# Kernel optimization log

Hardware: AMD Instinct MI355X
Metric: run time of the kernel (lower is better)

The kernel has to match this reference:

```python
import jax, jax.numpy as jnp
import numpy as np

H, KV, HD = 16, 8, 128           # heads, kv heads, head_dim
THETA, EPS = 1.0e6, 1e-6         # rope theta, rmsnorm eps
QMAX = 127.0                     # symmetric int8


def qdq(x):
    """Symmetric int8 fake quant-dequant along last dim (per-token / per-out-channel)."""
    s = jnp.maximum(jnp.max(jnp.abs(x), axis=-1, keepdims=True) / QMAX, 1e-8)
    q = jnp.clip(jnp.round(x / s), -QMAX, QMAX) * s
    return x + jax.lax.stop_gradient(q - x)  # STE


def rms_norm(x, w):
    v = jnp.mean(jnp.square(x.astype(jnp.float32)), axis=-1, keepdims=True)
    return (x.astype(jnp.float32) * jax.lax.rsqrt(v + EPS)).astype(x.dtype) * w


def rotate_half(x):
    x1, x2 = jnp.split(x, 2, axis=-1)
    return jnp.concatenate([-x2, x1], axis=-1)


def setup_inputs() -> dict:
    key = jax.random.key(0)
    ks = jax.random.split(key, 6)
    B, S, D = 1, 2048, 2048
    return {
        "hidden_states": jax.random.normal(ks[0], (B, S, D), jnp.float32),
        "Wq": jax.random.normal(ks[1], (H * HD, D), jnp.float32) * 0.02,
        "Wk": jax.random.normal(ks[2], (KV * HD, D), jnp.float32) * 0.02,
        "Wv": jax.random.normal(ks[3], (KV * HD, D), jnp.float32) * 0.02,
        "Wo": jax.random.normal(ks[4], (D, H * HD), jnp.float32) * 0.02,
        "q_norm_w": jnp.ones((HD,), jnp.float32),
        "k_norm_w": jnp.ones((HD,), jnp.float32),
        "position_ids": jnp.arange(S, dtype=jnp.int32)[None, :],
    }


def reference(hidden_states, Wq, Wk, Wv, Wo, q_norm_w, k_norm_w, position_ids):
    B, S, D = hidden_states.shape
    xq = qdq(hidden_states)                                  # per-token act quant (shared input)
    q = (xq @ qdq(Wq).T).reshape(B, S, H, HD).transpose(0, 2, 1, 3)   # [B,H,S,hd]
    k = (xq @ qdq(Wk).T).reshape(B, S, KV, HD).transpose(0, 2, 1, 3)  # [B,KV,S,hd]
    v = (xq @ qdq(Wv).T).reshape(B, S, KV, HD).transpose(0, 2, 1, 3)

    q = rms_norm(q, q_norm_w)
    k = rms_norm(k, k_norm_w)

    # rotary embeddings
    inv = 1.0 / (THETA ** (jnp.arange(0, HD, 2, dtype=jnp.float32) / HD))
    freqs = position_ids.astype(jnp.float32)[..., None] * inv          # [B,S,hd/2]
    emb = jnp.concatenate([freqs, freqs], axis=-1)                     # [B,S,hd]
    cos = jnp.cos(emb)[:, None].astype(q.dtype)                        # [B,1,S,hd]
    sin = jnp.sin(emb)[:, None].astype(q.dtype)
    q = q * cos + rotate_half(q) * sin
    k = k * cos + rotate_half(k) * sin

    # qkt_matmul.quant_x1 / quant_x2
    q = qdq(q)
    k = qdq(k)

    # GQA repeat
    g = H // KV
    k = jnp.repeat(k, g, axis=1)
    v = jnp.repeat(v, g, axis=1)

    scores = jnp.einsum("bhqd,bhkd->bhqk", q, k) * (HD ** -0.5)       # [B,H,S,S]
    causal = jnp.tril(jnp.ones((S, S), bool))
    scores = jnp.where(causal[None, None], scores, jnp.float32(-1e9))
    p = jax.nn.softmax(scores.astype(jnp.float32), axis=-1).astype(q.dtype)

    # pv_matmul.quant_x1 / quant_x2
    p = qdq(p)
    v = qdq(v)
    attn = jnp.einsum("bhqk,bhkd->bhqd", p, v)                        # [B,H,S,hd]
    attn = attn.transpose(0, 2, 1, 3).reshape(B, S, H * HD)
    return qdq(attn) @ qdq(Wo).T
```

## Files before the change

kernel.cpp:

```cpp
#include <hip/hip_runtime.h>
#include <math.h>

#define NH 16
#define NKV 8
#define HDIM 128
#define SEQ 2048
#define DMODEL 2048

typedef int   v4i __attribute__((ext_vector_type(4)));
typedef float v4f __attribute__((ext_vector_type(4)));
typedef _Float16 v8h __attribute__((ext_vector_type(8)));

static constexpr float SM_SCALE = 0.08838834764831843f;

#define GLOBP(p) (__attribute__((address_space(1))) void*)(p)
#define LDSP(p)  (__attribute__((address_space(3))) void*)(p)
#define ASYNC16(g, l) __builtin_amdgcn_global_load_lds(GLOBP(g), LDSP(l), 16, 0, 0)


__device__ __forceinline__ unsigned short f2h_bits(float x) {
    _Float16 h = (_Float16)x;
    return __builtin_bit_cast(unsigned short, h);
}

__global__ __launch_bounds__(256) void quant_rope_k(const float* __restrict__ hidden,
        const float* __restrict__ Wq, const float* __restrict__ Wk,
        const float* __restrict__ Wv, const float* __restrict__ Wo,
        const int* __restrict__ pos_ids,
        signed char* __restrict__ out, float* __restrict__ scale,
        float* __restrict__ ct, float* __restrict__ st) {
    int p = blockIdx.x;
    if (p >= 512) {
        int t = (p - 512) * 4 + (threadIdx.x >> 6);
        int fi = threadIdx.x & 63;
        float inv = 1.0f / (float)pow(1.0e6, (double)fi / 64.0);
        float fr = (float)pos_ids[t] * inv;
        float sn, c;
        sincosf(fr, &sn, &c);
        ct[t * 64 + fi] = c;
        st[t * 64 + fi] = sn;
        return;
    }
    int row0g = p * 16;
    const float* in; int lr0;
    if (row0g < 2048)      { in = hidden; lr0 = row0g; }
    else if (row0g < 4096) { in = Wq; lr0 = row0g - 2048; }
    else if (row0g < 5120) { in = Wk; lr0 = row0g - 4096; }
    else if (row0g < 6144) { in = Wv; lr0 = row0g - 5120; }
    else                   { in = Wo; lr0 = row0g - 6144; }
    const int cols = 2048;
    int tid = threadIdx.x;
    __shared__ float srow[16];
    int r = tid >> 4, l16 = tid & 15;
    const float4* x4 = (const float4*)(in + (size_t)(lr0 + r) * cols);
    float amax = 0.f;
    for (int c4 = l16; c4 < (cols >> 2); c4 += 16) {
        float4 v = x4[c4];
        amax = fmaxf(amax, fmaxf(fmaxf(fabsf(v.x), fabsf(v.y)),
                                 fmaxf(fabsf(v.z), fabsf(v.w))));
    }
#pragma unroll
    for (int m = 1; m <= 8; m <<= 1) amax = fmaxf(amax, __shfl_xor(amax, m));
    if (l16 == 0) {
        float s = fmaxf(amax / 127.0f, 1e-8f);
        srow[r] = s;
        scale[row0g + r] = s;
    }
    __syncthreads();
    int total = (cols >> 4) * 16;
    size_t obase = (size_t)p * 32768;
    for (int idx = tid; idx < total; idx += 256) {
        int f = idx >> 6, q = (idx >> 4) & 3, rr = idx & 15;
        const float* src = in + (size_t)(lr0 + rr) * cols + f * 64 + q * 16;
        float s = srow[rr];
        unsigned int wds[4];
#pragma unroll
        for (int g = 0; g < 4; ++g) {
            float4 v = *(const float4*)(src + g * 4);
            int b0 = (int)fminf(fmaxf(rintf(v.x / s), -127.f), 127.f);
            int b1 = (int)fminf(fmaxf(rintf(v.y / s), -127.f), 127.f);
            int b2 = (int)fminf(fmaxf(rintf(v.z / s), -127.f), 127.f);
            int b3 = (int)fminf(fmaxf(rintf(v.w / s), -127.f), 127.f);
            wds[g] = (b0 & 255) | ((b1 & 255) << 8) | ((b2 & 255) << 16) | ((b3 & 255) << 24);
        }
        *(uint4*)(out + obase + (size_t)idx * 16) =
            make_uint4(wds[0], wds[1], wds[2], wds[3]);
    }
}

__global__ __launch_bounds__(256) void row_quant_red_k(const float* __restrict__ attn2,
        const float* __restrict__ pp, const float* __restrict__ zb,
        signed char* __restrict__ out, float* __restrict__ scale) {
    int row0 = blockIdx.x * 16;
    bool corr = (row0 >= 1024);
    int tid = threadIdx.x;
    __shared__ float srow[16];
    __shared__ float spvt[16][17];
    if (corr) {
        int r = tid >> 4, h = tid & 15;
        int row = row0 + r;
        int t16 = (row >> 6) - 16, rr = row & 63;
        float z0 = zb[(((size_t)h * 16 + t16) * 2 + 0) * 64 + rr];
        float z1 = zb[(((size_t)h * 16 + t16) * 2 + 1) * 64 + rr];
        spvt[r][h] = fmaxf((1.0f / (z0 + z1)) / 127.0f, 1e-8f);
    }
    __syncthreads();
    int r = tid >> 4, l16 = tid & 15;
    int row = row0 + r;
    const float4* x4 = (const float4*)(attn2 + (size_t)row * 2048);
    size_t ppr = corr ? ((((size_t)(row >> 6) - 16) * 64 + (row & 63)) * 128) : 0;
    float amax = 0.f;
    for (int c4 = l16; c4 < 512; c4 += 16) {
        float4 v = x4[c4];
        if (corr) {
            int h = c4 >> 5;
            int j = (c4 & 31) * 4;
            float4 pv = *(const float4*)&pp[(size_t)h * 16 * 64 * 128 + ppr + j];
            float s = spvt[r][h];
            v.x = (v.x + pv.x) * s; v.y = (v.y + pv.y) * s;
            v.z = (v.z + pv.z) * s; v.w = (v.w + pv.w) * s;
        }
        amax = fmaxf(amax, fmaxf(fmaxf(fabsf(v.x), fabsf(v.y)),
                                 fmaxf(fabsf(v.z), fabsf(v.w))));
    }
#pragma unroll
    for (int m = 1; m <= 8; m <<= 1) amax = fmaxf(amax, __shfl_xor(amax, m));
    if (l16 == 0) {
        float s = fmaxf(amax / 127.0f, 1e-8f);
        srow[r] = s;
        scale[row0 + r] = s;
    }
    __syncthreads();
    size_t obase = ((size_t)(row0 >> 4) * 32) << 10;
    for (int idx = tid; idx < 2048; idx += 256) {
        int f = idx >> 6, q = (idx >> 4) & 3, rr16 = idx & 15;
        int rowb = row0 + rr16;
        int colb = f * 64 + q * 16;
        const float* src = attn2 + (size_t)rowb * 2048 + colb;
        float s = srow[rr16];
        int h = f >> 1;
        float sp = corr ? spvt[rr16][h] : 0.f;
        size_t ppb = corr ? ((size_t)h * 16 * 64 * 128
                     + (((size_t)(rowb >> 6) - 16) * 64 + (rowb & 63)) * 128 + (colb & 127)) : 0;
        unsigned int wds[4];
#pragma unroll
        for (int g = 0; g < 4; ++g) {
            float4 v = *(const float4*)(src + g * 4);
            if (corr) {
                float4 pv = *(const float4*)&pp[ppb + g * 4];
                v.x = (v.x + pv.x) * sp; v.y = (v.y + pv.y) * sp;
                v.z = (v.z + pv.z) * sp; v.w = (v.w + pv.w) * sp;
            }
            int b0 = (int)fminf(fmaxf(rintf(v.x / s), -127.f), 127.f);
            int b1 = (int)fminf(fmaxf(rintf(v.y / s), -127.f), 127.f);
            int b2 = (int)fminf(fmaxf(rintf(v.z / s), -127.f), 127.f);
            int b3 = (int)fminf(fmaxf(rintf(v.w / s), -127.f), 127.f);
            wds[g] = (b0 & 255) | ((b1 & 255) << 8) | ((b2 & 255) << 16) | ((b3 & 255) << 24);
        }
        *(uint4*)(out + obase + (size_t)idx * 16) =
            make_uint4(wds[0], wds[1], wds[2], wds[3]);
    }
}

__global__ __launch_bounds__(256, 3) void gemm_o_k(const signed char* __restrict__ A,
        const float* __restrict__ sa, const signed char* __restrict__ B,
        const float* __restrict__ sb, float* __restrict__ C, int M, int N, int K) {
    __shared__ __align__(16) signed char lsA[3][8192];
    __shared__ __align__(16) signed char lsB[3][4096];
    int tid = threadIdx.x;
    int w = tid >> 6, l = tid & 63;
    int wr = w >> 1, wc = w & 1;
    int lrow = l & 15;
    int m0 = blockIdx.y * 128, n0 = blockIdx.x * 64;
    int kb6 = K >> 6;
    v4i acc[4][2];
#pragma unroll
    for (int i = 0; i < 4; ++i)
#pragma unroll
        for (int j = 0; j < 2; ++j) acc[i][j] = (v4i){0, 0, 0, 0};

    auto stage = [&](int buf, int k6) {
#pragma unroll
        for (int a = 0; a < 2; ++a) {
            int f = a * 4 + w;
            ASYNC16(A + (((size_t)(((m0 >> 4) + f) * kb6 + k6)) << 10) + l * 16,
                    lsA[buf] + f * 1024);
        }
        ASYNC16(B + (((size_t)(((n0 >> 4) + w) * kb6 + k6)) << 10) + l * 16,
                lsB[buf] + w * 1024);
    };

    stage(0, 0);
    if (kb6 > 1) {
        stage(1, 1);
        asm volatile("s_waitcnt vmcnt(3)" ::: "memory");
    } else {
        asm volatile("s_waitcnt vmcnt(0)" ::: "memory");
    }
    __builtin_amdgcn_s_barrier();
    for (int t = 0; t < kb6; ++t) {
        if (t + 2 < kb6) stage((t + 2) % 3, t + 2);
        int cur = t % 3;
        v4i af[4], bf[2];
#pragma unroll
        for (int i = 0; i < 4; ++i) af[i] = *(const v4i*)(lsA[cur] + (wr * 4 + i) * 1024 + l * 16);
#pragma unroll
        for (int j = 0; j < 2; ++j) bf[j] = *(const v4i*)(lsB[cur] + (wc * 2 + j) * 1024 + l * 16);
#pragma unroll
        for (int i = 0; i < 4; ++i)
#pragma unroll
            for (int j = 0; j < 2; ++j)
                acc[i][j] = __builtin_amdgcn_mfma_i32_16x16x64_i8(af[i], bf[j], acc[i][j], 0, 0, 0);
        if (t + 2 < kb6) asm volatile("s_waitcnt vmcnt(3)" ::: "memory");
        else             asm volatile("s_waitcnt vmcnt(0)" ::: "memory");
        __builtin_amdgcn_s_barrier();
    }
    int r0 = m0 + wr * 64, c0 = n0 + wc * 32;
    int lg = l >> 4;
    float sbv[2];
#pragma unroll
    for (int j = 0; j < 2; ++j) sbv[j] = sb[c0 + j * 16 + lrow];
#pragma unroll
    for (int i = 0; i < 4; ++i) {
        float4 s4 = *(const float4*)(sa + r0 + i * 16 + lg * 4);
        float sav[4] = {s4.x, s4.y, s4.z, s4.w};
#pragma unroll
        for (int j = 0; j < 2; ++j) {
#pragma unroll
            for (int reg = 0; reg < 4; ++reg) {
                int rr = r0 + i * 16 + lg * 4 + reg;
                C[(size_t)rr * N + c0 + j * 16 + lrow] = (float)acc[i][j][reg] * (sav[reg] * sbv[j]);
            }
        }
    }
}

__global__ __launch_bounds__(256, 2) void gemm_qkv_k(const signed char* __restrict__ A,
        const float* __restrict__ sa, const signed char* __restrict__ B,
        const float* __restrict__ sb,
        const float* __restrict__ qw, const float* __restrict__ kw,
        const float* __restrict__ ct, const float* __restrict__ st,
        signed char* __restrict__ q_i8, float* __restrict__ sq,
        signed char* __restrict__ k_i8, float* __restrict__ sk,
        unsigned short* __restrict__ vtT) {
    __shared__ __align__(16) char smem[68608];
    signed char (*lsA)[8192] = (signed char(*)[8192])smem;
    signed char (*lsB)[8192] = (signed char(*)[8192])(smem + 24576);
    float (*tile)[132] = (float(*)[132])smem;
    float* srow = (float*)(smem + 67584);
    int tid = threadIdx.x;
    int w = tid >> 6, l = tid & 63;
    int wr = w >> 1, wc = w & 1;
    int lrow = l & 15, lg = l >> 4;
    int m0 = blockIdx.y * 128, n0 = blockIdx.x * 128;
    const int kb6 = 32;
    v4i acc[4][4];
#pragma unroll
    for (int i = 0; i < 4; ++i)
#pragma unroll
        for (int j = 0; j < 4; ++j) acc[i][j] = (v4i){0, 0, 0, 0};

    auto stage = [&](int buf, int k6) {
#pragma unroll
        for (int a = 0; a < 2; ++a) {
            int f = a * 4 + w;
            ASYNC16(A + (((size_t)(((m0 >> 4) + f) * kb6 + k6)) << 10) + l * 16,
                    lsA[buf] + f * 1024);
            ASYNC16(B + (((size_t)(((n0 >> 4) + f) * kb6 + k6)) << 10) + l * 16,
                    lsB[buf] + f * 1024);
        }
    };

    stage(0, 0);
    stage(1, 1);
    asm volatile("s_waitcnt vmcnt(4)" ::: "memory");
    __builtin_amdgcn_s_barrier();
    for (int t = 0; t < kb6; ++t) {
        if (t + 2 < kb6) stage((t + 2) % 3, t + 2);
        int cur = t % 3;
        v4i af[4], bf[4];
#pragma unroll
        for (int i = 0; i < 4; ++i) af[i] = *(const v4i*)(lsA[cur] + (wr * 4 + i) * 1024 + l * 16);
#pragma unroll
        for (int j = 0; j < 4; ++j) bf[j] = *(const v4i*)(lsB[cur] + (wc * 4 + j) * 1024 + l * 16);
#pragma unroll
        for (int i = 0; i < 4; ++i)
#pragma unroll
            for (int j = 0; j < 4; ++j)
                acc[i][j] = __builtin_amdgcn_mfma_i32_16x16x64_i8(af[i], bf[j], acc[i][j], 0, 0, 0);
        if (t + 2 < kb6) asm volatile("s_waitcnt vmcnt(4)" ::: "memory");
        else             asm volatile("s_waitcnt vmcnt(0)" ::: "memory");
        __builtin_amdgcn_s_barrier();
    }
    {
        int c0 = n0 + wc * 64;
        float sbv[4];
#pragma unroll
        for (int j = 0; j < 4; ++j) sbv[j] = sb[c0 + j * 16 + lrow];
#pragma unroll
        for (int i = 0; i < 4; ++i) {
            float4 s4 = *(const float4*)(sa + m0 + wr * 64 + i * 16 + lg * 4);
            float sav[4] = {s4.x, s4.y, s4.z, s4.w};
#pragma unroll
            for (int j = 0; j < 4; ++j)
#pragma unroll
                for (int reg = 0; reg < 4; ++reg)
                    tile[wr * 64 + i * 16 + lg * 4 + reg][wc * 64 + j * 16 + lrow] =
                        (float)acc[i][j][reg] * (sav[reg] * sbv[j]);
        }
    }
    __syncthreads();
    int slot = n0 >> 7;
    if (slot < 24) {
        const float* wn = (slot < 16) ? qw : kw;
        signed char* dst8 = (slot < 16) ? q_i8 + (size_t)slot * (SEQ * 128)
                                        : k_i8 + (size_t)(slot - 16) * (SEQ * 128);
        float* sdst = (slot < 16) ? sq + (size_t)slot * SEQ : sk + (size_t)(slot - 16) * SEQ;
        float wn0 = wn[l], wn1 = wn[l + 64];
        for (int it = 0; it < 32; ++it) {
            int tl = it * 4 + w;
            int t = m0 + tl;
            float x0 = tile[tl][l];
            float x1 = tile[tl][l + 64];
            float ss = x0 * x0 + x1 * x1;
#pragma unroll
            for (int m = 1; m <= 32; m <<= 1) ss += __shfl_xor(ss, m);
            float rs = 1.0f / sqrtf(ss / 128.0f + 1e-6f);
            x0 = (x0 * rs) * wn0;
            x1 = (x1 * rs) * wn1;
            float cth = ct[t * 64 + l];
            float sth = st[t * 64 + l];
            float nx0 = x0 * cth - x1 * sth;
            float nx1 = x1 * cth + x0 * sth;
            float amax = fmaxf(fabsf(nx0), fabsf(nx1));
#pragma unroll
            for (int m = 1; m <= 32; m <<= 1) amax = fmaxf(amax, __shfl_xor(amax, m));
            float s = fmaxf(amax / 127.0f, 1e-8f);
            float q0 = fminf(fmaxf(rintf(nx0 / s), -127.f), 127.f);
            float q1 = fminf(fmaxf(rintf(nx1 / s), -127.f), 127.f);
            size_t ta0 = (size_t)(((t >> 4) * 2) << 10)
                       + (size_t)((((l >> 4) & 3) << 8) + ((t & 15) << 4) + (l & 15));
            dst8[ta0] = (signed char)(int)q0;
            dst8[ta0 + 1024] = (signed char)(int)q1;
            if (l == 0) sdst[t] = s;
        }
    } else {
        int kv = slot - 24;
        for (int it = 0; it < 32; ++it) {
            int tl = it * 4 + w;
            float x0 = tile[tl][l];
            float x1 = tile[tl][l + 64];
            float amax = fmaxf(fabsf(x0), fabsf(x1));
#pragma unroll
            for (int m = 1; m <= 32; m <<= 1) amax = fmaxf(amax, __shfl_xor(amax, m));
            if (l == 0) srow[tl] = fmaxf(amax / 127.0f, 1e-8f);
        }
        __syncthreads();
        int d = tid >> 1, th = (tid & 1) * 32;
        size_t base = (size_t)kv * (SEQ * 128);
#pragma unroll
        for (int kbl = 0; kbl < 2; ++kbl) {
            int kb = (m0 >> 6) + kbl;
#pragma unroll
            for (int j = 0; j < 32; j += 2) {
                int t64 = th + j;
                int tg = kbl * 64 + t64;
                float s0 = srow[tg], s1 = srow[tg + 1];
                float a = fminf(fmaxf(rintf(tile[tg][d] / s0), -127.f), 127.f) * s0;
                float b = fminf(fmaxf(rintf(tile[tg + 1][d] / s1), -127.f), 127.f) * s1;
                unsigned int ua = f2h_bits(a), ub = f2h_bits(b);
                int off = kb * 8192 + ((d >> 4) * 2 + ((t64 >> 5) & 1)) * 512
                        + (((d & 15) + (((t64 >> 3) & 3) << 4)) << 3) + (t64 & 7);
                *(unsigned int*)(vtT + base + off) = ua | (ub << 16);
            }
        }
    }
}

__global__ __launch_bounds__(256, 4) void attn_p1_k(const signed char* __restrict__ q_i8,
        const float* __restrict__ sq, const signed char* __restrict__ k_i8,
        const float* __restrict__ sk, float* __restrict__ mm) {
    int bx = blockIdx.x, hp = blockIdx.y;
    int qb = 31 - (bx >> 2), c = bx & 3;
    int nch = (qb + 8) >> 3;
    if (c >= nch) return;
    int q0 = qb * 64;
    int kb0 = c * 8, kb1 = min((c + 1) * 8, qb + 1);
    int tid = threadIdx.x, w = tid >> 6, l = tid & 63;
    int lrow = l & 15, lg = l >> 4;
    int h0 = hp * 2, h1 = h0 + 1;

    const signed char* qtA = q_i8 + (size_t)h0 * (SEQ * 128)
                           + ((size_t)((((q0 >> 4) + w) * 2)) << 10) + l * 16;
    const signed char* qtB = qtA + (size_t)(SEQ * 128);
    v4i qfA0 = *(const v4i*)(qtA), qfA1 = *(const v4i*)(qtA + 1024);
    v4i qfB0 = *(const v4i*)(qtB), qfB1 = *(const v4i*)(qtB + 1024);
    float4 sA = *(const float4*)(sq + (size_t)h0 * SEQ + q0 + w * 16 + lg * 4);
    float4 sB = *(const float4*)(sq + (size_t)h1 * SEQ + q0 + w * 16 + lg * 4);
    float sqrA[4] = {sA.x, sA.y, sA.z, sA.w};
    float sqrB[4] = {sB.x, sB.y, sB.z, sB.w};
    const signed char* kbase = k_i8 + (size_t)hp * (SEQ * 128);
    const float* skb = sk + (size_t)hp * SEQ;

    float mA[4], mB[4];
#pragma unroll
    for (int r = 0; r < 4; ++r) { mA[r] = -1e30f; mB[r] = -1e30f; }

    v4i ka[8], kn[8];
    float skc[4], skn[4];
    auto loadK = [&](v4i* dst, float* sdst, int k0) {
#pragma unroll
        for (int f = 0; f < 8; ++f)
            dst[f] = *(const v4i*)(kbase + ((size_t)((k0 >> 4) * 2 + f) << 10) + l * 16);
#pragma unroll
        for (int j = 0; j < 4; ++j) sdst[j] = skb[k0 + j * 16 + lrow];
    };

    loadK(ka, skc, kb0 * 64);
    for (int kb = kb0; kb < kb1; ++kb) {
        if (kb + 1 < kb1) loadK(kn, skn, (kb + 1) * 64);
        int k0 = kb * 64;
        v4i sciA[4], sciB[4];
#pragma unroll
        for (int j = 0; j < 4; ++j) {
            v4i z = {0, 0, 0, 0};
            v4i tA = __builtin_amdgcn_mfma_i32_16x16x64_i8(qfA0, ka[j * 2], z, 0, 0, 0);
            sciA[j] = __builtin_amdgcn_mfma_i32_16x16x64_i8(qfA1, ka[j * 2 + 1], tA, 0, 0, 0);
            v4i tB = __builtin_amdgcn_mfma_i32_16x16x64_i8(qfB0, ka[j * 2], z, 0, 0, 0);
            sciB[j] = __builtin_amdgcn_mfma_i32_16x16x64_i8(qfB1, ka[j * 2 + 1], tB, 0, 0, 0);
        }
#pragma unroll
        for (int reg = 0; reg < 4; ++reg) {
            int r = q0 + w * 16 + lg * 4 + reg;
#pragma unroll
            for (int j = 0; j < 4; ++j) {
                bool ok = (k0 + j * 16 + lrow <= r);
                float ss = skc[j] * SM_SCALE;
                float svA = ((float)sciA[j][reg] * sqrA[reg]) * ss;
                float svB = ((float)sciB[j][reg] * sqrB[reg]) * ss;
                mA[reg] = fmaxf(mA[reg], ok ? svA : -1e30f);
                mB[reg] = fmaxf(mB[reg], ok ? svB : -1e30f);
            }
        }
        if (kb + 1 < kb1) {
#pragma unroll
            for (int f = 0; f < 8; ++f) ka[f] = kn[f];
#pragma unroll
            for (int j = 0; j < 4; ++j) skc[j] = skn[j];
        }
    }
#pragma unroll
    for (int reg = 0; reg < 4; ++reg) {
#pragma unroll
        for (int mask = 1; mask <= 8; mask <<= 1) {
            mA[reg] = fmaxf(mA[reg], __shfl_xor(mA[reg], mask));
            mB[reg] = fmaxf(mB[reg], __shfl_xor(mB[reg], mask));
        }
    }
    if (lrow == 0) {
        size_t bA = ((size_t)(h0 * 32 + qb) * 4 + c) * 64;
        size_t bB = ((size_t)(h1 * 32 + qb) * 4 + c) * 64;
#pragma unroll
        for (int reg = 0; reg < 4; ++reg) {
            mm[bA + w * 16 + lg * 4 + reg] = mA[reg];
            mm[bB + w * 16 + lg * 4 + reg] = mB[reg];
        }
    }
}

__global__ __launch_bounds__(256, 2) void attn_p2_k(const signed char* __restrict__ q_i8,
        const float* __restrict__ sq, const signed char* __restrict__ k_i8,
        const float* __restrict__ sk, const unsigned short* __restrict__ vtT,
        const float* __restrict__ mm, float* __restrict__ attn2, float* __restrict__ pp,
        float* __restrict__ zb) {
    __shared__ __align__(16) unsigned short vlds[3][8192];
    __shared__ __align__(16) signed char klds[2][8192];
    __shared__ __align__(16) unsigned short plds[4096];
    __shared__ __align__(16) float slds[1024];
    int bx = blockIdx.x, hp = blockIdx.y;
    int qb = 31 - (bx >> 1), c = bx & 1;
    int nch2 = (qb >= 16) ? 2 : 1;
    if (c >= nch2) return;
    int q0 = qb * 64;
    int kb0 = c * 16, kb1 = min((c + 1) * 16, qb + 1);
    int tid = threadIdx.x, w = tid >> 6, l = tid & 63;
    int lrow = l & 15, lg = l >> 4;
    int h0 = hp * 2, h1 = h0 + 1;

    const signed char* qtA = q_i8 + (size_t)h0 * (SEQ * 128)
                           + ((size_t)((((q0 >> 4) + w) * 2)) << 10) + l * 16;
    const signed char* qtB = qtA + (size_t)(SEQ * 128);
    v4i qfA0 = *(const v4i*)(qtA), qfA1 = *(const v4i*)(qtA + 1024);
    v4i qfB0 = *(const v4i*)(qtB), qfB1 = *(const v4i*)(qtB + 1024);
    float4 sA = *(const float4*)(sq + (size_t)h0 * SEQ + q0 + w * 16 + lg * 4);
    float4 sB = *(const float4*)(sq + (size_t)h1 * SEQ + q0 + w * 16 + lg * 4);
    float sqrA[4] = {sA.x, sA.y, sA.z, sA.w};
    float sqrB[4] = {sB.x, sB.y, sB.z, sB.w};

    int nch1 = (qb + 8) >> 3;
    float mfA[4], mfB[4];
#pragma unroll
    for (int reg = 0; reg < 4; ++reg) {
        int r = w * 16 + lg * 4 + reg;
        float MA = -1e30f, MB = -1e30f;
        for (int c1 = 0; c1 < nch1; ++c1) {
            MA = fmaxf(MA, mm[((size_t)(h0 * 32 + qb) * 4 + c1) * 64 + r]);
            MB = fmaxf(MB, mm[((size_t)(h1 * 32 + qb) * 4 + c1) * 64 + r]);
        }
        mfA[reg] = MA; mfB[reg] = MB;
    }

    const signed char* kbase = k_i8 + (size_t)hp * (SEQ * 128);
    const float* skb = sk + (size_t)hp * SEQ;
    const unsigned short* vt = vtT + (size_t)hp * (SEQ * 128);

    auto issueV = [&](int kb) {
        unsigned short* vb = &vlds[kb % 3][0];
#pragma unroll
        for (int a = 0; a < 4; ++a) {
            int fv = a * 4 + w;
            ASYNC16(vt + (size_t)kb * 8192 + fv * 512 + l * 8, vb + fv * 512);
        }
    };
    auto issueK = [&](int kb) {
        signed char* kbuf = &klds[kb & 1][0];
#pragma unroll
        for (int a = 0; a < 2; ++a) {
            int f = a * 4 + w;
            ASYNC16(kbase + ((size_t)(kb * 8 + f) << 10) + l * 16, kbuf + f * 1024);
        }
    };

    v4f accA[8], accB[8];
#pragma unroll
    for (int jd = 0; jd < 8; ++jd) {
        accA[jd] = (v4f){0.f, 0.f, 0.f, 0.f};
        accB[jd] = (v4f){0.f, 0.f, 0.f, 0.f};
    }
    float ztA[4] = {0.f, 0.f, 0.f, 0.f};
    float ztB[4] = {0.f, 0.f, 0.f, 0.f};

    ASYNC16(skb + kb0 * 64 + w * 256 + l * 4, (char*)slds + w * 1024);
    issueK(kb0);
    issueV(kb0);
    if (kb0 + 1 < kb1) {
        issueV(kb0 + 1);
        asm volatile("s_waitcnt vmcnt(4)" ::: "memory");
    } else {
        asm volatile("s_waitcnt vmcnt(0)" ::: "memory");
    }
    __builtin_amdgcn_s_barrier();

    for (int kb = kb0; kb < kb1; ++kb) {
        int k0 = kb * 64;
        if (kb + 1 < kb1) issueK(kb + 1);
        if (kb + 2 < kb1) issueV(kb + 2);
        v4i ka[8];
#pragma unroll
        for (int f = 0; f < 8; ++f)
            ka[f] = *(const v4i*)(&klds[kb & 1][0] + f * 1024 + l * 16);
        float skc[4];
#pragma unroll
        for (int j = 0; j < 4; ++j) skc[j] = slds[(kb - kb0) * 64 + j * 16 + lrow];
        v4i sciA[4], sciB[4];
#pragma unroll
        for (int j = 0; j < 4; ++j) {
            v4i z = {0, 0, 0, 0};
            v4i tA = __builtin_amdgcn_mfma_i32_16x16x64_i8(qfA0, ka[j * 2], z, 0, 0, 0);
            sciA[j] = __builtin_amdgcn_mfma_i32_16x16x64_i8(qfA1, ka[j * 2 + 1], tA, 0, 0, 0);
            v4i tB = __builtin_amdgcn_mfma_i32_16x16x64_i8(qfB0, ka[j * 2], z, 0, 0, 0);
            sciB[j] = __builtin_amdgcn_mfma_i32_16x16x64_i8(qfB1, ka[j * 2 + 1], tB, 0, 0, 0);
        }
#pragma unroll
        for (int reg = 0; reg < 4; ++reg) {
            int rq = lg * 4 + reg;
            int r = q0 + w * 16 + rq;
#pragma unroll
            for (int j = 0; j < 4; ++j) {
                int cc = j * 16 + lrow;
                float pd = 0.f;
                if (k0 + cc <= r) {
                    float sv = ((float)sciA[j][reg] * (sqrA[reg] * skc[j])) * SM_SCALE;
                    float e = __expf(sv - mfA[reg]);
                    ztA[reg] += e;
                    pd = fminf(rintf(127.0f * e), 127.f);
                }
                plds[(w * 2 + (cc >> 5)) * 512 + (rq + 16 * ((cc >> 3) & 3)) * 8 + (cc & 7)] =
                    f2h_bits(pd);
            }
        }
        v8h pfA0 = *(const v8h*)(plds + (w * 2 + 0) * 512 + l * 8);
        v8h pfA1 = *(const v8h*)(plds + (w * 2 + 1) * 512 + l * 8);
#pragma unroll
        for (int reg = 0; reg < 4; ++reg) {
            int rq = lg * 4 + reg;
            int r = q0 + w * 16 + rq;
#pragma unroll
            for (int j = 0; j < 4; ++j) {
                int cc = j * 16 + lrow;
                float pd = 0.f;
                if (k0 + cc <= r) {
                    float sv = ((float)sciB[j][reg] * (sqrB[reg] * skc[j])) * SM_SCALE;
                    float e = __expf(sv - mfB[reg]);
                    ztB[reg] += e;
                    pd = fminf(rintf(127.0f * e), 127.f);
                }
                plds[(w * 2 + (cc >> 5)) * 512 + (rq + 16 * ((cc >> 3) & 3)) * 8 + (cc & 7)] =
                    f2h_bits(pd);
            }
        }
        v8h pfB0 = *(const v8h*)(plds + (w * 2 + 0) * 512 + l * 8);
        v8h pfB1 = *(const v8h*)(plds + (w * 2 + 1) * 512 + l * 8);
        const unsigned short* vb = &vlds[kb % 3][0];
#pragma unroll
        for (int jd = 0; jd < 8; ++jd) {
            v8h vh0 = *(const v8h*)(vb + (jd * 2 + 0) * 512 + l * 8);
            v8h vh1 = *(const v8h*)(vb + (jd * 2 + 1) * 512 + l * 8);
            v4f tA = accA[jd];
            tA = __builtin_amdgcn_mfma_f32_16x16x32_f16(pfA0, vh0, tA, 0, 0, 0);
            tA = __builtin_amdgcn_mfma_f32_16x16x32_f16(pfA1, vh1, tA, 0, 0, 0);
            accA[jd] = tA;
            v4f tB = accB[jd];
            tB = __builtin_amdgcn_mfma_f32_16x16x32_f16(pfB0, vh0, tB, 0, 0, 0);
            tB = __builtin_amdgcn_mfma_f32_16x16x32_f16(pfB1, vh1, tB, 0, 0, 0);
            accB[jd] = tB;
        }
        if (kb + 2 < kb1) asm volatile("s_waitcnt vmcnt(4)" ::: "memory");
        else              asm volatile("s_waitcnt vmcnt(0)" ::: "memory");
        __builtin_amdgcn_s_barrier();
    }
#pragma unroll
    for (int reg = 0; reg < 4; ++reg) {
#pragma unroll
        for (int mask = 1; mask <= 8; mask <<= 1) {
            ztA[reg] += __shfl_xor(ztA[reg], mask);
            ztB[reg] += __shfl_xor(ztB[reg], mask);
        }
    }
    if (qb < 16) {
        float spA[4], spB[4];
#pragma unroll
        for (int reg = 0; reg < 4; ++reg) {
            spA[reg] = fmaxf((1.0f / ztA[reg]) / 127.0f, 1e-8f);
            spB[reg] = fmaxf((1.0f / ztB[reg]) / 127.0f, 1e-8f);
        }
#pragma unroll
        for (int jd = 0; jd < 8; ++jd)
#pragma unroll
            for (int reg = 0; reg < 4; ++reg) {
                int r = q0 + w * 16 + lg * 4 + reg;
                attn2[(size_t)r * DMODEL + h0 * HDIM + jd * 16 + lrow] = accA[jd][reg] * spA[reg];
                attn2[(size_t)r * DMODEL + h1 * HDIM + jd * 16 + lrow] = accB[jd][reg] * spB[reg];
            }
    } else {
        if (c == 0) {
#pragma unroll
            for (int jd = 0; jd < 8; ++jd)
#pragma unroll
                for (int reg = 0; reg < 4; ++reg) {
                    int r = q0 + w * 16 + lg * 4 + reg;
                    attn2[(size_t)r * DMODEL + h0 * HDIM + jd * 16 + lrow] = accA[jd][reg];
                    attn2[(size_t)r * DMODEL + h1 * HDIM + jd * 16 + lrow] = accB[jd][reg];
                }
        } else {
#pragma unroll
            for (int jd = 0; jd < 8; ++jd)
#pragma unroll
                for (int reg = 0; reg < 4; ++reg) {
                    int rr = w * 16 + lg * 4 + reg;
                    pp[(((size_t)h0 * 16 + (qb - 16)) * 64 + rr) * 128 + jd * 16 + lrow] = accA[jd][reg];
                    pp[(((size_t)h1 * 16 + (qb - 16)) * 64 + rr) * 128 + jd * 16 + lrow] = accB[jd][reg];
                }
        }
        if (lrow == 0) {
            size_t zA = (((size_t)h0 * 16 + (qb - 16)) * 2 + c) * 64;
            size_t zB = (((size_t)h1 * 16 + (qb - 16)) * 2 + c) * 64;
#pragma unroll
            for (int reg = 0; reg < 4; ++reg) {
                zb[zA + w * 16 + lg * 4 + reg] = ztA[reg];
                zb[zB + w * 16 + lg * 4 + reg] = ztB[reg];
            }
        }
    }
}

extern "C" void kernel_launch(void* const* d_in, const int* in_sizes, int n_in,
                              void* d_out, int out_size, void* d_ws, size_t ws_size,
                              hipStream_t stream) {
    (void)in_sizes; (void)n_in; (void)out_size; (void)ws_size;
    const float* hidden = (const float*)d_in[0];
    const float* Wq = (const float*)d_in[1];
    const float* Wk = (const float*)d_in[2];
    const float* Wv = (const float*)d_in[3];
    const float* Wo = (const float*)d_in[4];
    const float* qw = (const float*)d_in[5];
    const float* kw = (const float*)d_in[6];
    const int* pos = (const int*)d_in[7];
    float* out = (float*)d_out;
    char* ws = (char*)d_ws;

    const size_t MB = 1024 * 1024;
    signed char* x_i8  = (signed char*)(ws);
    signed char* wq_i8 = (signed char*)(ws + 4 * MB);
    signed char* wo_i8 = (signed char*)(ws + 12 * MB);
    signed char* q_i8  = (signed char*)(ws + 16 * MB);
    signed char* k_i8  = (signed char*)(ws + 20 * MB);
    float* sx  = (float*)(ws + 22 * MB);
    float* swq = sx + 2048;
    float* swo = sx + 6144;
    float* sq  = sx + 8192;
    float* sk  = sq + NH * SEQ;
    float* sa  = sk + NKV * SEQ;
    float* ct  = (float*)(ws + 22 * MB + 512 * 1024);
    float* st  = (float*)(ws + 22 * MB + 1024 * 1024);
    float* attn2 = (float*)(ws + 32 * MB);
    float* pp    = (float*)(ws + 48 * MB);
    unsigned short* vtT = (unsigned short*)(ws + 56 * MB);
    float* mm    = (float*)(ws + 60 * MB);
    float* zb    = (float*)(ws + 60 * MB + 512 * 1024);
    signed char* a_i8 = x_i8;

    quant_rope_k<<<1024, 256, 0, stream>>>(hidden, Wq, Wk, Wv, Wo, pos, x_i8, sx, ct, st);

    gemm_qkv_k<<<dim3(32, 16), 256, 0, stream>>>(x_i8, sx, wq_i8, swq, qw, kw, ct, st,
                                                 q_i8, sq, k_i8, sk, vtT);

    attn_p1_k<<<dim3(128, 8), 256, 0, stream>>>(q_i8, sq, k_i8, sk, mm);
    attn_p2_k<<<dim3(64, 8), 256, 0, stream>>>(q_i8, sq, k_i8, sk, vtT, mm, attn2, pp, zb);

    row_quant_red_k<<<128, 256, 0, stream>>>(attn2, pp, zb, a_i8, sa);
    gemm_o_k<<<dim3(32, 16), 256, 0, stream>>>(a_i8, sa, wo_i8, swo, out, 2048, 2048, 2048);
}
```

Baseline: 190.4 us.

## Fuse two-pass attention into single-pass online softmax with chunk merging

Removes the separate max-finding kernel, which recomputed QK^T just to get row maxima. The main attention kernel now keeps a running max per row and rescales its accumulators and partial sums whenever a new key block raises that max. Each split chunk writes its (max, sum) pair, and the row-quant reduction kernel merges the two chunks with exp weights. The cost is extra exp and rescale work inside the loop. There is also a numerics risk: P is now quantized against the running max instead of the final row max, so the int8 rounding of P no longer matches the reference exactly.

```diff
diff --git a/kernel.cpp b/kernel.cpp
--- a/kernel.cpp
+++ b/kernel.cpp
@@ -95,14 +95,19 @@
     bool corr = (row0 >= 1024);
     int tid = threadIdx.x;
     __shared__ float srow[16];
-    __shared__ float spvt[16][17];
+    __shared__ float4 spvt[16][17];
     if (corr) {
         int r = tid >> 4, h = tid & 15;
         int row = row0 + r;
         int t16 = (row >> 6) - 16, rr = row & 63;
-        float z0 = zb[(((size_t)h * 16 + t16) * 2 + 0) * 64 + rr];
-        float z1 = zb[(((size_t)h * 16 + t16) * 2 + 1) * 64 + rr];
-        spvt[r][h] = fmaxf((1.0f / (z0 + z1)) / 127.0f, 1e-8f);
+        const float2* zb2 = (const float2*)zb;
+        float2 a0 = zb2[(((size_t)h * 16 + t16) * 2 + 0) * 64 + rr];
+        float2 a1 = zb2[(((size_t)h * 16 + t16) * 2 + 1) * 64 + rr];
+        float M = fmaxf(a0.x, a1.x);
+        float w0 = __expf(a0.x - M), w1 = __expf(a1.x - M);
+        float Zt = a0.y * w0 + a1.y * w1;
+        float spv = fmaxf((1.0f / Zt) / 127.0f, 1e-8f);
+        spvt[r][h] = make_float4(w0, w1, spv, 0.f);
     }
     __syncthreads();
     int r = tid >> 4, l16 = tid & 15;
@@ -116,9 +121,11 @@
             int h = c4 >> 5;
             int j = (c4 & 31) * 4;
             float4 pv = *(const float4*)&pp[(size_t)h * 16 * 64 * 128 + ppr + j];
-            float s = spvt[r][h];
-            v.x = (v.x + pv.x) * s; v.y = (v.y + pv.y) * s;
-            v.z = (v.z + pv.z) * s; v.w = (v.w + pv.w) * s;
+            float4 wz = spvt[r][h];
+            v.x = (v.x * wz.x + pv.x * wz.y) * wz.z;
+            v.y = (v.y * wz.x + pv.y * wz.y) * wz.z;
+            v.z = (v.z * wz.x + pv.z * wz.y) * wz.z;
+            v.w = (v.w * wz.x + pv.w * wz.y) * wz.z;
         }
         amax = fmaxf(amax, fmaxf(fmaxf(fabsf(v.x), fabsf(v.y)),
                                  fmaxf(fabsf(v.z), fabsf(v.w))));
@@ -139,7 +146,7 @@
         const float* src = attn2 + (size_t)rowb * 2048 + colb;
         float s = srow[rr16];
         int h = f >> 1;
-        float sp = corr ? spvt[rr16][h] : 0.f;
+        float4 wz = corr ? spvt[rr16][h] : make_float4(1.f, 0.f, 0.f, 0.f);
         size_t ppb = corr ? ((size_t)h * 16 * 64 * 128
                      + (((size_t)(rowb >> 6) - 16) * 64 + (rowb & 63)) * 128 + (colb & 127)) : 0;
         unsigned int wds[4];
@@ -148,8 +155,10 @@
             float4 v = *(const float4*)(src + g * 4);
             if (corr) {
                 float4 pv = *(const float4*)&pp[ppb + g * 4];
-                v.x = (v.x + pv.x) * sp; v.y = (v.y + pv.y) * sp;
-                v.z = (v.z + pv.z) * sp; v.w = (v.w + pv.w) * sp;
+                v.x = (v.x * wz.x + pv.x * wz.y) * wz.z;
+                v.y = (v.y * wz.x + pv.y * wz.y) * wz.z;
+                v.z = (v.z * wz.x + pv.z * wz.y) * wz.z;
+                v.w = (v.w * wz.x + pv.w * wz.y) * wz.z;
             }
             int b0 = (int)fminf(fmaxf(rintf(v.x / s), -127.f), 127.f);
             int b1 = (int)fminf(fmaxf(rintf(v.y / s), -127.f), 127.f);
@@ -377,102 +386,10 @@
     }
 }
 
-__global__ __launch_bounds__(256, 4) void attn_p1_k(const signed char* __restrict__ q_i8,
-        const float* __restrict__ sq, const signed char* __restrict__ k_i8,
-        const float* __restrict__ sk, float* __restrict__ mm) {
-    int bx = blockIdx.x, hp = blockIdx.y;
-    int qb = 31 - (bx >> 2), c = bx & 3;
-    int nch = (qb + 8) >> 3;
-    if (c >= nch) return;
-    int q0 = qb * 64;
-    int kb0 = c * 8, kb1 = min((c + 1) * 8, qb + 1);
-    int tid = threadIdx.x, w = tid >> 6, l = tid & 63;
-    int lrow = l & 15, lg = l >> 4;
-    int h0 = hp * 2, h1 = h0 + 1;
-
-    const signed char* qtA = q_i8 + (size_t)h0 * (SEQ * 128)
-                           + ((size_t)((((q0 >> 4) + w) * 2)) << 10) + l * 16;
-    const signed char* qtB = qtA + (size_t)(SEQ * 128);
-    v4i qfA0 = *(const v4i*)(qtA), qfA1 = *(const v4i*)(qtA + 1024);
-    v4i qfB0 = *(const v4i*)(qtB), qfB1 = *(const v4i*)(qtB + 1024);
-    float4 sA = *(const float4*)(sq + (size_t)h0 * SEQ + q0 + w * 16 + lg * 4);
-    float4 sB = *(const float4*)(sq + (size_t)h1 * SEQ + q0 + w * 16 + lg * 4);
-    float sqrA[4] = {sA.x, sA.y, sA.z, sA.w};
-    float sqrB[4] = {sB.x, sB.y, sB.z, sB.w};
-    const signed char* kbase = k_i8 + (size_t)hp * (SEQ * 128);
-    const float* skb = sk + (size_t)hp * SEQ;
-
-    float mA[4], mB[4];
-#pragma unroll
-    for (int r = 0; r < 4; ++r) { mA[r] = -1e30f; mB[r] = -1e30f; }
-
-    v4i ka[8], kn[8];
-    float skc[4], skn[4];
-    auto loadK = [&](v4i* dst, float* sdst, int k0) {
-#pragma unroll
-        for (int f = 0; f < 8; ++f)
-            dst[f] = *(const v4i*)(kbase + ((size_t)((k0 >> 4) * 2 + f) << 10) + l * 16);
-#pragma unroll
-        for (int j = 0; j < 4; ++j) sdst[j] = skb[k0 + j * 16 + lrow];
-    };
-
-    loadK(ka, skc, kb0 * 64);
-    for (int kb = kb0; kb < kb1; ++kb) {
-        if (kb + 1 < kb1) loadK(kn, skn, (kb + 1) * 64);
-        int k0 = kb * 64;
-        v4i sciA[4], sciB[4];
-#pragma unroll
-        for (int j = 0; j < 4; ++j) {
-            v4i z = {0, 0, 0, 0};
-            v4i tA = __builtin_amdgcn_mfma_i32_16x16x64_i8(qfA0, ka[j * 2], z, 0, 0, 0);
-            sciA[j] = __builtin_amdgcn_mfma_i32_16x16x64_i8(qfA1, ka[j * 2 + 1], tA, 0, 0, 0);
-            v4i tB = __builtin_amdgcn_mfma_i32_16x16x64_i8(qfB0, ka[j * 2], z, 0, 0, 0);
-            sciB[j] = __builtin_amdgcn_mfma_i32_16x16x64_i8(qfB1, ka[j * 2 + 1], tB, 0, 0, 0);
-        }
-#pragma unroll
-        for (int reg = 0; reg < 4; ++reg) {
-            int r = q0 + w * 16 + lg * 4 + reg;
-#pragma unroll
-            for (int j = 0; j < 4; ++j) {
-                bool ok = (k0 + j * 16 + lrow <= r);
-                float ss = skc[j] * SM_SCALE;
-                float svA = ((float)sciA[j][reg] * sqrA[reg]) * ss;
-                float svB = ((float)sciB[j][reg] * sqrB[reg]) * ss;
-                mA[reg] = fmaxf(mA[reg], ok ? svA : -1e30f);
-                mB[reg] = fmaxf(mB[reg], ok ? svB : -1e30f);
-            }
-        }
-        if (kb + 1 < kb1) {
-#pragma unroll
-            for (int f = 0; f < 8; ++f) ka[f] = kn[f];
-#pragma unroll
-            for (int j = 0; j < 4; ++j) skc[j] = skn[j];
-        }
-    }
-#pragma unroll
-    for (int reg = 0; reg < 4; ++reg) {
-#pragma unroll
-        for (int mask = 1; mask <= 8; mask <<= 1) {
-            mA[reg] = fmaxf(mA[reg], __shfl_xor(mA[reg], mask));
-            mB[reg] = fmaxf(mB[reg], __shfl_xor(mB[reg], mask));
-        }
-    }
-    if (lrow == 0) {
-        size_t bA = ((size_t)(h0 * 32 + qb) * 4 + c) * 64;
-        size_t bB = ((size_t)(h1 * 32 + qb) * 4 + c) * 64;
-#pragma unroll
-        for (int reg = 0; reg < 4; ++reg) {
-            mm[bA + w * 16 + lg * 4 + reg] = mA[reg];
-            mm[bB + w * 16 + lg * 4 + reg] = mB[reg];
-        }
-    }
-}
-
-__global__ __launch_bounds__(256, 2) void attn_p2_k(const signed char* __restrict__ q_i8,
+__global__ __launch_bounds__(256, 2) void attn_k(const signed char* __restrict__ q_i8,
         const float* __restrict__ sq, const signed char* __restrict__ k_i8,
         const float* __restrict__ sk, const unsigned short* __restrict__ vtT,
-        const float* __restrict__ mm, float* __restrict__ attn2, float* __restrict__ pp,
-        float* __restrict__ zb) {
+        float* __restrict__ attn2, float* __restrict__ pp, float* __restrict__ zb) {
     __shared__ __align__(16) unsigned short vlds[3][8192];
     __shared__ __align__(16) signed char klds[2][8192];
     __shared__ __align__(16) unsigned short plds[4096];
@@ -497,19 +414,6 @@
     float sqrA[4] = {sA.x, sA.y, sA.z, sA.w};
     float sqrB[4] = {sB.x, sB.y, sB.z, sB.w};
 
-    int nch1 = (qb + 8) >> 3;
-    float mfA[4], mfB[4];
-#pragma unroll
-    for (int reg = 0; reg < 4; ++reg) {
-        int r = w * 16 + lg * 4 + reg;
-        float MA = -1e30f, MB = -1e30f;
-        for (int c1 = 0; c1 < nch1; ++c1) {
-            MA = fmaxf(MA, mm[((size_t)(h0 * 32 + qb) * 4 + c1) * 64 + r]);
-            MB = fmaxf(MB, mm[((size_t)(h1 * 32 + qb) * 4 + c1) * 64 + r]);
-        }
-        mfA[reg] = MA; mfB[reg] = MB;
-    }
-
     const signed char* kbase = k_i8 + (size_t)hp * (SEQ * 128);
     const float* skb = sk + (size_t)hp * SEQ;
     const unsigned short* vt = vtT + (size_t)hp * (SEQ * 128);
@@ -539,6 +443,9 @@
     }
     float ztA[4] = {0.f, 0.f, 0.f, 0.f};
     float ztB[4] = {0.f, 0.f, 0.f, 0.f};
+    float mA[4], mB[4];
+#pragma unroll
+    for (int r = 0; r < 4; ++r) { mA[r] = -1e30f; mB[r] = -1e30f; }
 
     ASYNC16(skb + kb0 * 64 + w * 256 + l * 4, (char*)slds + w * 1024);
     issueK(kb0);
@@ -571,17 +478,61 @@
             v4i tB = __builtin_amdgcn_mfma_i32_16x16x64_i8(qfB0, ka[j * 2], z, 0, 0, 0);
             sciB[j] = __builtin_amdgcn_mfma_i32_16x16x64_i8(qfB1, ka[j * 2 + 1], tB, 0, 0, 0);
         }
+        float svA[4][4], svB[4][4];
+        float tmA[4], tmB[4];
+#pragma unroll
+        for (int reg = 0; reg < 4; ++reg) { tmA[reg] = -1e30f; tmB[reg] = -1e30f; }
+#pragma unroll
+        for (int reg = 0; reg < 4; ++reg) {
+            int r = q0 + w * 16 + lg * 4 + reg;
+#pragma unroll
+            for (int j = 0; j < 4; ++j) {
+                int cc = j * 16 + lrow;
+                bool ok = (k0 + cc <= r);
+                float ss = skc[j] * SM_SCALE;
+                svA[reg][j] = ok ? ((float)sciA[j][reg] * sqrA[reg]) * ss : -1e30f;
+                svB[reg][j] = ok ? ((float)sciB[j][reg] * sqrB[reg]) * ss : -1e30f;
+                tmA[reg] = fmaxf(tmA[reg], svA[reg][j]);
+                tmB[reg] = fmaxf(tmB[reg], svB[reg][j]);
+            }
+        }
+#pragma unroll
+        for (int reg = 0; reg < 4; ++reg) {
+#pragma unroll
+            for (int mask = 1; mask <= 8; mask <<= 1) {
+                tmA[reg] = fmaxf(tmA[reg], __shfl_xor(tmA[reg], mask));
+                tmB[reg] = fmaxf(tmB[reg], __shfl_xor(tmB[reg], mask));
+            }
+        }
+        float efA[4], efB[4];
+#pragma unroll
+        for (int reg = 0; reg < 4; ++reg) {
+            float mnA = fmaxf(mA[reg], tmA[reg]);
+            efA[reg] = __expf(mA[reg] - mnA);
+            mA[reg] = mnA;
+            ztA[reg] *= efA[reg];
+            float mnB = fmaxf(mB[reg], tmB[reg]);
+            efB[reg] = __expf(mB[reg] - mnB);
+            mB[reg] = mnB;
+            ztB[reg] *= efB[reg];
+        }
+        v4f efvA = {efA[0], efA[1], efA[2], efA[3]};
+        v4f efvB = {efB[0], efB[1], efB[2], efB[3]};
+#pragma unroll
+        for (int jd = 0; jd < 8; ++jd) {
+            accA[jd] *= efvA;
+            accB[jd] *= efvB;
+        }
 #pragma unroll
         for (int reg = 0; reg < 4; ++reg) {
             int rq = lg * 4 + reg;
-            int r = q0 + w * 16 + rq;
 #pragma unroll
             for (int j = 0; j < 4; ++j) {
                 int cc = j * 16 + lrow;
                 float pd = 0.f;
-                if (k0 + cc <= r) {
-                    float sv = ((float)sciA[j][reg] * (sqrA[reg] * skc[j])) * SM_SCALE;
-                    float e = __expf(sv - mfA[reg]);
+                float sv = svA[reg][j];
+                if (sv > -5e29f) {
+                    float e = __expf(sv - mA[reg]);
                     ztA[reg] += e;
                     pd = fminf(rintf(127.0f * e), 127.f);
                 }
@@ -594,14 +545,13 @@
 #pragma unroll
         for (int reg = 0; reg < 4; ++reg) {
             int rq = lg * 4 + reg;
-            int r = q0 + w * 16 + rq;
 #pragma unroll
             for (int j = 0; j < 4; ++j) {
                 int cc = j * 16 + lrow;
                 float pd = 0.f;
-                if (k0 + cc <= r) {
-                    float sv = ((float)sciB[j][reg] * (sqrB[reg] * skc[j])) * SM_SCALE;
-                    float e = __expf(sv - mfB[reg]);
+                float sv = svB[reg][j];
+                if (sv > -5e29f) {
+                    float e = __expf(sv - mB[reg]);
                     ztB[reg] += e;
                     pd = fminf(rintf(127.0f * e), 127.f);
                 }
@@ -673,12 +623,13 @@
                 }
         }
         if (lrow == 0) {
+            float2* zb2 = (float2*)zb;
             size_t zA = (((size_t)h0 * 16 + (qb - 16)) * 2 + c) * 64;
             size_t zB = (((size_t)h1 * 16 + (qb - 16)) * 2 + c) * 64;
 #pragma unroll
             for (int reg = 0; reg < 4; ++reg) {
-                zb[zA + w * 16 + lg * 4 + reg] = ztA[reg];
-                zb[zB + w * 16 + lg * 4 + reg] = ztB[reg];
+                zb2[zA + w * 16 + lg * 4 + reg] = make_float2(mA[reg], ztA[reg]);
+                zb2[zB + w * 16 + lg * 4 + reg] = make_float2(mB[reg], ztB[reg]);
             }
         }
     }
@@ -716,8 +667,7 @@
     float* attn2 = (float*)(ws + 32 * MB);
     float* pp    = (float*)(ws + 48 * MB);
     unsigned short* vtT = (unsigned short*)(ws + 56 * MB);
-    float* mm    = (float*)(ws + 60 * MB);
-    float* zb    = (float*)(ws + 60 * MB + 512 * 1024);
+    float* zb    = (float*)(ws + 60 * MB);
     signed char* a_i8 = x_i8;
 
     quant_rope_k<<<1024, 256, 0, stream>>>(hidden, Wq, Wk, Wv, Wo, pos, x_i8, sx, ct, st);
@@ -725,8 +675,7 @@
     gemm_qkv_k<<<dim3(32, 16), 256, 0, stream>>>(x_i8, sx, wq_i8, swq, qw, kw, ct, st,
                                                  q_i8, sq, k_i8, sk, vtT);
 
-    attn_p1_k<<<dim3(128, 8), 256, 0, stream>>>(q_i8, sq, k_i8, sk, mm);
-    attn_p2_k<<<dim3(64, 8), 256, 0, stream>>>(q_i8, sq, k_i8, sk, vtT, mm, attn2, pp, zb);
+    attn_k<<<dim3(64, 8), 256, 0, stream>>>(q_i8, sq, k_i8, sk, vtT, attn2, pp, zb);
 
     row_quant_red_k<<<128, 256, 0, stream>>>(attn2, pp, zb, a_i8, sa);
     gemm_o_k<<<dim3(32, 16), 256, 0, stream>>>(a_i8, sa, wo_i8, swo, out, 2048, 2048, 2048);
```

Result: no change. 187.0 us (-1.8%).
